# Kernel optimization log

Hardware: AMD Instinct MI355X
Metric: run time of the kernel (lower is better)

Reference implementation:

```python
import jax, jax.numpy as jnp
import numpy as np

B, T, E, H = 2, 4096, 768, 12
D = E // H  # head_dim = 64


def setup_inputs() -> dict:
    key = jax.random.key(0)
    ks = jax.random.split(key, 9)
    s = 1.0 / np.sqrt(E)
    return {
        "x": jax.random.normal(ks[0], (B, T, E), dtype=jnp.float32),
        "wq": jax.random.normal(ks[1], (E, E), dtype=jnp.float32) * s,
        "bq": jnp.zeros((E,), dtype=jnp.float32),
        "wk": jax.random.normal(ks[2], (E, E), dtype=jnp.float32) * s,
        "bk": jnp.zeros((E,), dtype=jnp.float32),
        "wv": jax.random.normal(ks[3], (E, E), dtype=jnp.float32) * s,
        "bv": jnp.zeros((E,), dtype=jnp.float32),
        "wo": jax.random.normal(ks[4], (E, E), dtype=jnp.float32) * s,
        "bo": jnp.zeros((E,), dtype=jnp.float32),
    }


def reference(x, wq, bq, wk, bk, wv, bv, wo, bo):
    # Linear projections (torch Linear: x @ W.T + b; weights here stored as (in,out))
    q = x @ wq + bq  # (B,T,E)
    k = x @ wk + bk
    v = x @ wv + bv

    def split(t):
        return t.reshape(B, T, H, D).transpose(0, 2, 1, 3)  # (B,H,T,D)

    q, k, v = split(q), split(k), split(v)
    scale = 1.0 / np.sqrt(D).astype(np.float32)
    scores = jnp.einsum("bhtd,bhsd->bhts", q, k) * scale  # (B,H,T,T)
    causal = jnp.tril(jnp.ones((T, T), dtype=bool))
    scores = jnp.where(causal, scores, -jnp.inf)
    attn = jax.nn.softmax(scores, axis=-1)
    out = jnp.einsum("bhts,bhsd->bhtd", attn, v)  # (B,H,T,D)
    out = out.transpose(0, 2, 1, 3).reshape(B, T, E)
    return out @ wo + bo
```

## Files before the change

### kernel.cpp

```cpp
#include <hip/hip_runtime.h>
#include <hip/hip_bf16.h>

#define TSEQ 4096
#define EMB 768
#define NH 12
#define DH 64
#define BT 8192
#define NROWS (24 * TSEQ)

typedef __attribute__((ext_vector_type(8))) short bf16x8;
typedef __attribute__((ext_vector_type(4))) float f32x4;

#define FENCE() asm volatile("" ::: "memory")

__device__ __forceinline__ f32x4 mfma16(bf16x8 a, bf16x8 b, f32x4 c) {
    return __builtin_amdgcn_mfma_f32_16x16x32_bf16(a, b, c, 0, 0, 0);
}

__device__ __forceinline__ void gload16(const void* g, void* l) {
    __builtin_amdgcn_global_load_lds((const __attribute__((address_space(1))) void*)g,
                                     (__attribute__((address_space(3))) void*)l, 16, 0, 0);
}

__global__ __launch_bounds__(256) void conv_all_k(const float* __restrict__ x,
                                                  __hip_bfloat16* __restrict__ xb,
                                                  const float* w0, const float* w1,
                                                  const float* w2, const float* w3,
                                                  __hip_bfloat16* o0, __hip_bfloat16* o1,
                                                  __hip_bfloat16* o2, __hip_bfloat16* o3) {
    __shared__ float tile[32][33];
    int bid = blockIdx.x;
    if (bid < 6144) {
        int i = (bid * 256 + threadIdx.x) * 4;
        float4 v = *(const float4*)(x + i);
        union { unsigned short u[4]; uint2 p; } o;
        __hip_bfloat16 t0 = __float2bfloat16(v.x); o.u[0] = *(unsigned short*)&t0;
        __hip_bfloat16 t1 = __float2bfloat16(v.y); o.u[1] = *(unsigned short*)&t1;
        __hip_bfloat16 t2 = __float2bfloat16(v.z); o.u[2] = *(unsigned short*)&t2;
        __hip_bfloat16 t3 = __float2bfloat16(v.w); o.u[3] = *(unsigned short*)&t3;
        *(uint2*)(xb + i) = o.p;
        return;
    }
    bid -= 6144;
    const int z = bid / 576, rr = bid % 576, by = rr / 24, bx = rr % 24;
    const float* w; __hip_bfloat16* o;
    switch (z) {
        case 0: w = w0; o = o0; break;
        case 1: w = w1; o = o1; break;
        case 2: w = w2; o = o2; break;
        default: w = w3; o = o3; break;
    }
    int tx = threadIdx.x & 31, ty = threadIdx.x >> 5;
    int kb = by * 32, nb = bx * 32;
    for (int i = 0; i < 32; i += 8)
        tile[ty + i][tx] = w[(size_t)(kb + ty + i) * EMB + nb + tx];
    __syncthreads();
    for (int i = 0; i < 32; i += 8)
        o[(size_t)(nb + ty + i) * EMB + kb + tx] = __float2bfloat16(tile[tx][ty + i]);
}

__device__ __forceinline__ void gemm_body(const __hip_bfloat16* __restrict__ A,
                                          const __hip_bfloat16* __restrict__ Wt,
                                          const float* __restrict__ bias,
                                          void* __restrict__ outp, int mode, float scale) {
    __shared__ alignas(16) char As[2][8192];
    __shared__ alignas(16) char Bs[2][8192];
    const int m0 = blockIdx.x * 128, n0 = blockIdx.y * 128;
    const int tid = threadIdx.x;
    const int lane = tid & 63, l15 = lane & 15, lg = lane >> 4;
    const int wave = tid >> 6, wm = wave >> 1, wn = wave & 1;
    const int swz = (l15 & 7) << 4;

    int mrow_[2]; int kelem_[2];
#pragma unroll
    for (int c = 0; c < 2; ++c) {
        int p = c * 4096 + tid * 16;
        int lrow = p >> 7, w = p & 127;
        int wp = w ^ ((lrow & 7) << 4);
        mrow_[c] = lrow + ((wp >> 6) & 1) * 64;
        kelem_[c] = (wp & 63) >> 1;
    }

    f32x4 acc[4][4];
    for (int i = 0; i < 4; ++i)
        for (int j = 0; j < 4; ++j) acc[i][j] = (f32x4){0.f, 0.f, 0.f, 0.f};

    auto stage = [&](int buf, int k0) {
#pragma unroll
        for (int c = 0; c < 2; ++c)
            gload16(A + (size_t)(m0 + mrow_[c]) * EMB + k0 + kelem_[c],
                    As[buf] + c * 4096 + wave * 1024);
#pragma unroll
        for (int c = 0; c < 2; ++c)
            gload16(Wt + (size_t)(n0 + mrow_[c]) * EMB + k0 + kelem_[c],
                    Bs[buf] + c * 4096 + wave * 1024);
    };

    stage(0, 0);
    const int NK = EMB / 32;
    for (int ks = 0; ks < NK; ++ks) {
        const int cur = ks & 1;
        asm volatile("s_waitcnt vmcnt(0)" ::: "memory");
        FENCE(); __builtin_amdgcn_s_barrier(); FENCE();
        if (ks + 1 < NK) stage(cur ^ 1, (ks + 1) * 32);
        bf16x8 af[4], bfv[4];
#pragma unroll
        for (int f = 0; f < 4; ++f)
            af[f] = *(const bf16x8*)(As[cur] + (f * 16 + l15) * 128 + ((wm * 64 + lg * 16) ^ swz));
#pragma unroll
        for (int f = 0; f < 4; ++f)
            bfv[f] = *(const bf16x8*)(Bs[cur] + (f * 16 + l15) * 128 + ((wn * 64 + lg * 16) ^ swz));
        __builtin_amdgcn_s_setprio(1);
#pragma unroll
        for (int i = 0; i < 4; ++i)
#pragma unroll
            for (int j = 0; j < 4; ++j)
                acc[i][j] = mfma16(af[i], bfv[j], acc[i][j]);
        __builtin_amdgcn_s_setprio(0);
    }

#pragma unroll
    for (int i = 0; i < 4; ++i) {
#pragma unroll
        for (int j = 0; j < 4; ++j) {
            const int n = n0 + wn * 64 + j * 16 + l15;
            const float bv = bias[n];
            const int mbase = m0 + wm * 64 + i * 16 + lg * 4;
#pragma unroll
            for (int r = 0; r < 4; ++r) {
                const int m = mbase + r;
                const float val = (acc[i][j][r] + bv) * scale;
                if (mode == 2) {
                    ((float*)outp)[(size_t)m * EMB + n] = val;
                } else {
                    const int b = m >> 12, t = m & (TSEQ - 1);
                    const int h = n >> 6, d = n & 63;
                    size_t addr;
                    if (mode == 0) addr = ((size_t)(b * NH + h) * TSEQ + t) * DH + d;
                    else           addr = ((size_t)(b * NH + h) * DH + d) * TSEQ + t;
                    ((__hip_bfloat16*)outp)[addr] = __float2bfloat16(val);
                }
            }
        }
    }
}

__global__ __launch_bounds__(256) void qkv_k(const __hip_bfloat16* __restrict__ xb,
                                             const __hip_bfloat16* __restrict__ wqT,
                                             const __hip_bfloat16* __restrict__ wkT,
                                             const __hip_bfloat16* __restrict__ wvT,
                                             const float* __restrict__ bq,
                                             const float* __restrict__ bk,
                                             const float* __restrict__ bv,
                                             __hip_bfloat16* __restrict__ qo,
                                             __hip_bfloat16* __restrict__ ko,
                                             __hip_bfloat16* __restrict__ vo) {
    const __hip_bfloat16* Wt; const float* bias; void* o; int mode; float scale;
    const float cq = 0.125f * 1.44269504089f;
    switch (blockIdx.z) {
        case 0:  Wt = wqT; bias = bq; o = qo; mode = 0; scale = cq;  break;
        case 1:  Wt = wkT; bias = bk; o = ko; mode = 0; scale = 1.f; break;
        default: Wt = wvT; bias = bv; o = vo; mode = 1; scale = 1.f; break;
    }
    gemm_body(xb, Wt, bias, o, mode, scale);
}

__global__ __launch_bounds__(256) void oproj64_k(const __hip_bfloat16* __restrict__ A,
                                                 const __hip_bfloat16* __restrict__ Wt,
                                                 const float* __restrict__ bias,
                                                 float* __restrict__ out) {
    __shared__ alignas(16) char As[2][4096];
    __shared__ alignas(16) char Bs[2][8192];
    const int m0 = blockIdx.x * 64, n0 = blockIdx.y * 128;
    const int tid = threadIdx.x;
    const int lane = tid & 63, l15 = lane & 15, lg = lane >> 4;
    const int wave = tid >> 6, wm = wave >> 1, wn = wave & 1;
    const int swz = (l15 & 7) << 4;

    int amrow, akelem;
    {
        int p = tid * 16;
        int lrow = p >> 7, w = p & 127;
        int wp = w ^ ((lrow & 7) << 4);
        amrow = lrow + ((wp >> 6) & 1) * 32;
        akelem = (wp & 63) >> 1;
    }
    int bnrow[2], bkelem[2];
#pragma unroll
    for (int c = 0; c < 2; ++c) {
        int p = c * 4096 + tid * 16;
        int lrow = p >> 7, w = p & 127;
        int wp = w ^ ((lrow & 7) << 4);
        bnrow[c] = lrow + ((wp >> 6) & 1) * 64;
        bkelem[c] = (wp & 63) >> 1;
    }

    f32x4 acc[2][4];
    for (int i = 0; i < 2; ++i)
        for (int j = 0; j < 4; ++j) acc[i][j] = (f32x4){0.f, 0.f, 0.f, 0.f};

    auto stage = [&](int buf, int k0) {
        gload16(A + (size_t)(m0 + amrow) * EMB + k0 + akelem,
                As[buf] + wave * 1024);
#pragma unroll
        for (int c = 0; c < 2; ++c)
            gload16(Wt + (size_t)(n0 + bnrow[c]) * EMB + k0 + bkelem[c],
                    Bs[buf] + c * 4096 + wave * 1024);
    };

    stage(0, 0);
    const int NK = EMB / 32;
    for (int ks = 0; ks < NK; ++ks) {
        const int cur = ks & 1;
        asm volatile("s_waitcnt vmcnt(0)" ::: "memory");
        FENCE(); __builtin_amdgcn_s_barrier(); FENCE();
        if (ks + 1 < NK) stage(cur ^ 1, (ks + 1) * 32);
        bf16x8 af[2], bfv[4];
#pragma unroll
        for (int f = 0; f < 2; ++f)
            af[f] = *(const bf16x8*)(As[cur] + (f * 16 + l15) * 128 + ((wm * 64 + lg * 16) ^ swz));
#pragma unroll
        for (int f = 0; f < 4; ++f)
            bfv[f] = *(const bf16x8*)(Bs[cur] + (f * 16 + l15) * 128 + ((wn * 64 + lg * 16) ^ swz));
        __builtin_amdgcn_s_setprio(1);
#pragma unroll
        for (int i = 0; i < 2; ++i)
#pragma unroll
            for (int j = 0; j < 4; ++j)
                acc[i][j] = mfma16(af[i], bfv[j], acc[i][j]);
        __builtin_amdgcn_s_setprio(0);
    }

#pragma unroll
    for (int i = 0; i < 2; ++i) {
#pragma unroll
        for (int j = 0; j < 4; ++j) {
            const int n = n0 + wn * 64 + j * 16 + l15;
            const float bv = bias[n];
            const int mbase = m0 + wm * 32 + i * 16 + lg * 4;
#pragma unroll
            for (int r = 0; r < 4; ++r)
                out[(size_t)(mbase + r) * EMB + n] = acc[i][j][r] + bv;
        }
    }
}

__global__ __launch_bounds__(256, 3) void attn_k(const __hip_bfloat16* __restrict__ qb,
                                                 const __hip_bfloat16* __restrict__ kb,
                                                 const __hip_bfloat16* __restrict__ vt,
                                                 __hip_bfloat16* __restrict__ opart,
                                                 float* __restrict__ lpart) {
    __shared__ alignas(16) char Ks[8192];
    __shared__ alignas(16) char Vs[8192];
    __shared__ alignas(16) char pbuf[4][2048];
    const int lane = threadIdx.x & 63, l15 = lane & 15, lg = lane >> 4;
    const int wave = threadIdx.x >> 6;
    const int bid = blockIdx.x;
    const int xcd = bid & 7, slot = bid >> 3;
    const int pair = slot & 31;
    const int parity = (slot >> 5) & 1;
    const int hgrp = slot >> 6;
    const int bh = xcd + hgrp * 8;
    const __hip_bfloat16* Qh = qb + (size_t)bh * TSEQ * DH;
    const __hip_bfloat16* Kh = kb + (size_t)bh * TSEQ * DH;
    const __hip_bfloat16* Vh = vt + (size_t)bh * DH * TSEQ;
    char* Pb = pbuf[wave];
    const int swz = (l15 & 7) << 4;
    const float M0 = 12.0f;

    bf16x8 ones8;
#pragma unroll
    for (int j = 0; j < 8; ++j) ones8[j] = (short)0x3F80;

    unsigned ka[8];
#pragma unroll
    for (int st = 0; st < 4; ++st)
#pragma unroll
        for (int ks = 0; ks < 2; ++ks)
            ka[st * 2 + ks] = (unsigned)((st * 16 + l15) * 128 + ((ks * 64 + lg * 16) ^ swz));
    char* pw[4]; char* pr[2];
#pragma unroll
    for (int st = 0; st < 4; ++st) pw[st] = Pb + l15 * 128 + ((st * 32 + lg * 8) ^ swz);
#pragma unroll
    for (int ks = 0; ks < 2; ++ks) pr[ks] = Pb + l15 * 128 + ((ks * 64 + lg * 16) ^ swz);
    const int dthr = wave * 16 + l15 - lg * 4;

    int r_[2], wp_[2];
#pragma unroll
    for (int c = 0; c < 2; ++c) {
        int p = c * 4096 + wave * 1024 + lane * 16;
        int r = p >> 7, w = p & 127;
        r_[c] = r;
        wp_[c] = (w ^ ((r & 7) << 4)) >> 1;
    }

    const int lo = pair, hi = 63 - pair;
    const int q0l = lo * 64 + wave * 16;
    const int q0h = hi * 64 + wave * 16;
    const int nsb = hi + 1;

    bf16x8 qh0 = *(const bf16x8*)(Qh + (size_t)(q0h + l15) * DH + lg * 8);
    bf16x8 qh1 = *(const bf16x8*)(Qh + (size_t)(q0h + l15) * DH + 32 + lg * 8);
    bf16x8 ql0 = *(const bf16x8*)(Qh + (size_t)(q0l + l15) * DH + lg * 8);
    bf16x8 ql1 = *(const bf16x8*)(Qh + (size_t)(q0l + l15) * DH + 32 + lg * 8);

    f32x4 oh[4], ol[4];
#pragma unroll
    for (int dt = 0; dt < 4; ++dt) { oh[dt] = (f32x4){0.f,0.f,0.f,0.f}; ol[dt] = (f32x4){0.f,0.f,0.f,0.f}; }
    f32x4 lh = (f32x4){0.f,0.f,0.f,0.f}, ll = (f32x4){0.f,0.f,0.f,0.f};

    const char* kg0 = (const char*)(Kh + (size_t)r_[0] * DH + wp_[0]) + parity * 8192;
    const char* kg1 = (const char*)(Kh + (size_t)r_[1] * DH + wp_[1]) + parity * 8192;
    const char* vg0 = (const char*)(Vh + (size_t)r_[0] * TSEQ + wp_[0]) + parity * 128;
    const char* vg1 = (const char*)(Vh + (size_t)r_[1] * TSEQ + wp_[1]) + parity * 128;

#define STAGE() do {                                                             \
    gload16(kg0, Ks + wave * 1024);                                              \
    gload16(kg1, Ks + 4096 + wave * 1024);                                       \
    gload16(vg0, Vs + wave * 1024);                                              \
    gload16(vg1, Vs + 4096 + wave * 1024);                                       \
    kg0 += 16384; kg1 += 16384; vg0 += 256; vg1 += 256;                          \
} while (0)

#define QKSM(KF, Q0, Q1, MASKB) do {                                             \
    f32x4 sa[4];                                                                 \
    __builtin_amdgcn_s_setprio(1);                                               \
    _Pragma("unroll")                                                            \
    for (int st = 0; st < 4; ++st) {                                             \
        f32x4 z = (f32x4){0.f, 0.f, 0.f, 0.f};                                   \
        z = mfma16(KF[st * 2 + 0], Q0, z);                                       \
        z = mfma16(KF[st * 2 + 1], Q1, z);                                       \
        sa[st] = z;                                                              \
    }                                                                            \
    __builtin_amdgcn_s_setprio(0);                                               \
    if (MASKB) {                                                                 \
        _Pragma("unroll")                                                        \
        for (int st = 0; st < 4; ++st)                                           \
            _Pragma("unroll")                                                    \
            for (int r = 0; r < 4; ++r)                                          \
                if (st * 16 + r > dthr) sa[st][r] = -INFINITY;                   \
    }                                                                            \
    _Pragma("unroll")                                                            \
    for (int st = 0; st < 4; ++st) {                                             \
        const float e0 = exp2f(sa[st][0] - M0);                                  \
        const float e1 = exp2f(sa[st][1] - M0);                                  \
        const float e2 = exp2f(sa[st][2] - M0);                                  \
        const float e3 = exp2f(sa[st][3] - M0);                                  \
        uint2 pkv;                                                               \
        asm("v_cvt_pk_bf16_f32 %0, %1, %2" : "=v"(pkv.x) : "v"(e0), "v"(e1));    \
        asm("v_cvt_pk_bf16_f32 %0, %1, %2" : "=v"(pkv.y) : "v"(e2), "v"(e3));    \
        *(uint2*)pw[st] = pkv;                                                   \
    }                                                                            \
} while (0)

#define PVU(VF, OV, LA) do {                                                     \
    bf16x8 pf0 = *(const bf16x8*)pr[0];                                          \
    bf16x8 pf1 = *(const bf16x8*)pr[1];                                          \
    __builtin_amdgcn_s_setprio(1);                                               \
    LA = mfma16(pf0, ones8, LA);                                                 \
    LA = mfma16(pf1, ones8, LA);                                                 \
    _Pragma("unroll")                                                            \
    for (int dt = 0; dt < 4; ++dt)                                               \
        OV[dt] = mfma16(pf0, VF[dt * 2 + 0], OV[dt]);                            \
    _Pragma("unroll")                                                            \
    for (int dt = 0; dt < 4; ++dt)                                               \
        OV[dt] = mfma16(pf1, VF[dt * 2 + 1], OV[dt]);                            \
    __builtin_amdgcn_s_setprio(0);                                               \
} while (0)

    STAGE();
    for (int sb = parity; sb < nsb; sb += 2) {
        const bool loact = (sb <= lo);
        asm volatile("s_waitcnt vmcnt(0)" ::: "memory");
        FENCE(); __builtin_amdgcn_s_barrier(); FENCE();
        bf16x8 kf[8];
#pragma unroll
        for (int i = 0; i < 8; ++i) kf[i] = *(const bf16x8*)(Ks + ka[i]);
        QKSM(kf, qh0, qh1, (sb == hi));
        bf16x8 vf[8];
#pragma unroll
        for (int i = 0; i < 8; ++i) vf[i] = *(const bf16x8*)(Vs + ka[i]);
        asm volatile("s_waitcnt lgkmcnt(0)" ::: "memory");
        FENCE(); __builtin_amdgcn_s_barrier(); FENCE();
        if (sb + 2 < nsb) STAGE();
        PVU(vf, oh, lh);
        if (loact) {
            FENCE();
            QKSM(kf, ql0, ql1, (sb == lo));
            asm volatile("s_waitcnt lgkmcnt(0)" ::: "memory");
            PVU(vf, ol, ll);
        }
    }

#undef PVU
#undef QKSM
#undef STAGE

    const size_t prow = ((size_t)parity * 24 + bh) * TSEQ;
    {
#pragma unroll
        for (int r = 0; r < 4; ++r) {
            const size_t base = (prow + q0h + lg * 4 + r) * DH;
#pragma unroll
            for (int dt = 0; dt < 4; ++dt)
                opart[base + dt * 16 + l15] = __float2bfloat16(oh[dt][r]);
        }
        if (l15 == 0) {
#pragma unroll
            for (int r = 0; r < 4; ++r) lpart[prow + q0h + lg * 4 + r] = lh[r];
        }
    }
    {
#pragma unroll
        for (int r = 0; r < 4; ++r) {
            const size_t base = (prow + q0l + lg * 4 + r) * DH;
#pragma unroll
            for (int dt = 0; dt < 4; ++dt)
                opart[base + dt * 16 + l15] = __float2bfloat16(ol[dt][r]);
        }
        if (l15 == 0) {
#pragma unroll
            for (int r = 0; r < 4; ++r) lpart[prow + q0l + lg * 4 + r] = ll[r];
        }
    }
}

__global__ __launch_bounds__(256) void comb_k(const __hip_bfloat16* __restrict__ opart,
                                              const float* __restrict__ lpart,
                                              __hip_bfloat16* __restrict__ ab) {
    const int idx = blockIdx.x * 256 + threadIdx.x;
    const int row = idx >> 3;
    const int d0 = (idx & 7) * 8;
    const int bh = row >> 12, qrow = row & 4095;
    const int b_ = bh / NH, h = bh % NH;
    bf16x8 a0 = *(const bf16x8*)(opart + (size_t)row * DH + d0);
    bf16x8 a1 = *(const bf16x8*)(opart + ((size_t)NROWS + row) * DH + d0);
    const float linv = 1.0f / (lpart[row] + lpart[NROWS + row]);
    union { unsigned short u[8]; uint4 v; } o;
#pragma unroll
    for (int j = 0; j < 8; ++j) {
        const float v0 = __uint_as_float(((unsigned)(unsigned short)a0[j]) << 16);
        const float v1 = __uint_as_float(((unsigned)(unsigned short)a1[j]) << 16);
        __hip_bfloat16 hb = __float2bfloat16((v0 + v1) * linv);
        o.u[j] = *(unsigned short*)&hb;
    }
    *(uint4*)(ab + ((size_t)(b_ * TSEQ + qrow)) * EMB + h * DH + d0) = o.v;
}

extern "C" void kernel_launch(void* const* d_in, const int* in_sizes, int n_in,
                              void* d_out, int out_size, void* d_ws, size_t ws_size,
                              hipStream_t stream) {
    (void)in_sizes; (void)n_in; (void)out_size; (void)ws_size;
    const float* x  = (const float*)d_in[0];
    const float* wq = (const float*)d_in[1];
    const float* bq = (const float*)d_in[2];
    const float* wk = (const float*)d_in[3];
    const float* bk = (const float*)d_in[4];
    const float* wv = (const float*)d_in[5];
    const float* bv = (const float*)d_in[6];
    const float* wo = (const float*)d_in[7];
    const float* bo = (const float*)d_in[8];
    float* out = (float*)d_out;

    char* ws = (char*)d_ws;
    size_t off = 0;
    auto alloc = [&](size_t bytes) {
        char* p = ws + off;
        off += (bytes + 255) & ~(size_t)255;
        return p;
    };
    __hip_bfloat16* xb   = (__hip_bfloat16*)alloc((size_t)BT * EMB * 2);
    __hip_bfloat16* qbf  = (__hip_bfloat16*)alloc((size_t)BT * EMB * 2);
    __hip_bfloat16* kbf  = (__hip_bfloat16*)alloc((size_t)BT * EMB * 2);
    __hip_bfloat16* vtb  = (__hip_bfloat16*)alloc((size_t)BT * EMB * 2);
    __hip_bfloat16* abf  = (__hip_bfloat16*)alloc((size_t)BT * EMB * 2);
    __hip_bfloat16* wqT  = (__hip_bfloat16*)alloc((size_t)EMB * EMB * 2);
    __hip_bfloat16* wkT  = (__hip_bfloat16*)alloc((size_t)EMB * EMB * 2);
    __hip_bfloat16* wvT  = (__hip_bfloat16*)alloc((size_t)EMB * EMB * 2);
    __hip_bfloat16* woT  = (__hip_bfloat16*)alloc((size_t)EMB * EMB * 2);
    __hip_bfloat16* opart = (__hip_bfloat16*)alloc((size_t)2 * NROWS * DH * 2);
    float*          lpart = (float*)alloc((size_t)2 * NROWS * 4);

    conv_all_k<<<6144 + 2304, 256, 0, stream>>>(x, xb, wq, wk, wv, wo, wqT, wkT, wvT, woT);
    qkv_k<<<dim3(64, 6, 3), 256, 0, stream>>>(xb, wqT, wkT, wvT, bq, bk, bv, qbf, kbf, vtb);
    attn_k<<<1536, 256, 0, stream>>>(qbf, kbf, vtb, opart, lpart);
    comb_k<<<NROWS * 8 / 256, 256, 0, stream>>>(opart, lpart, abf);
    oproj64_k<<<dim3(128, 6), 256, 0, stream>>>(abf, woT, bo, out);
}
```

Before: 183.7 us.

## Fuse split-KV combine into output projection and double-buffer K/V in attention

Removes the separate combine kernel: the output-projection GEMM now loads both partial attention outputs and their row sums, normalizes them, packs to bf16 and writes the A tile to LDS itself. This skips the write and re-read of the intermediate attention buffer and one launch. The cost is that the combine work is repeated for each of the 6 output column tiles, and the A tile now goes through registers instead of a direct global-to-LDS load. Separately, the attention kernel double-buffers its K/V LDS tiles, which removes the second barrier per iteration so the next block's loads can overlap compute, at the price of extra LDS that may reduce occupancy.

Measured after the change: 187.4 us. +2.0%, slower.

```diff
diff --git a/kernel.cpp b/kernel.cpp
--- a/kernel.cpp
+++ b/kernel.cpp
@@ -20,6 +20,10 @@
 __device__ __forceinline__ void gload16(const void* g, void* l) {
     __builtin_amdgcn_global_load_lds((const __attribute__((address_space(1))) void*)g,
                                      (__attribute__((address_space(3))) void*)l, 16, 0, 0);
+}
+
+__device__ __forceinline__ float bf2f(unsigned short u) {
+    return __uint_as_float(((unsigned)u) << 16);
 }
 
 __global__ __launch_bounds__(256) void conv_all_k(const float* __restrict__ x,
@@ -165,10 +169,11 @@
     gemm_body(xb, Wt, bias, o, mode, scale);
 }
 
-__global__ __launch_bounds__(256) void oproj64_k(const __hip_bfloat16* __restrict__ A,
-                                                 const __hip_bfloat16* __restrict__ Wt,
-                                                 const float* __restrict__ bias,
-                                                 float* __restrict__ out) {
+__global__ __launch_bounds__(256) void oprojc_k(const __hip_bfloat16* __restrict__ opart,
+                                                const float* __restrict__ lpart,
+                                                const __hip_bfloat16* __restrict__ Wt,
+                                                const float* __restrict__ bias,
+                                                float* __restrict__ out) {
     __shared__ alignas(16) char As[2][4096];
     __shared__ alignas(16) char Bs[2][8192];
     const int m0 = blockIdx.x * 64, n0 = blockIdx.y * 128;
@@ -185,6 +190,8 @@
         amrow = lrow + ((wp >> 6) & 1) * 32;
         akelem = (wp & 63) >> 1;
     }
+    const int m = m0 + amrow;
+    const int b_ = m >> 12, t = m & (TSEQ - 1);
     int bnrow[2], bkelem[2];
 #pragma unroll
     for (int c = 0; c < 2; ++c) {
@@ -200,8 +207,20 @@
         for (int j = 0; j < 4; ++j) acc[i][j] = (f32x4){0.f, 0.f, 0.f, 0.f};
 
     auto stage = [&](int buf, int k0) {
-        gload16(A + (size_t)(m0 + amrow) * EMB + k0 + akelem,
-                As[buf] + wave * 1024);
+        const int h = k0 >> 6;
+        const int d0 = (k0 & 63) + akelem;
+        const size_t orow = ((size_t)(b_ * NH + h)) * TSEQ + t;
+        bf16x8 a0 = *(const bf16x8*)(opart + orow * DH + d0);
+        bf16x8 a1 = *(const bf16x8*)(opart + ((size_t)NROWS + orow) * DH + d0);
+        const float li = 1.0f / (lpart[orow] + lpart[NROWS + orow]);
+        union { unsigned w[4]; uint4 v; } pk;
+#pragma unroll
+        for (int jp = 0; jp < 4; ++jp) {
+            const float e0 = (bf2f((unsigned short)a0[2 * jp]) + bf2f((unsigned short)a1[2 * jp])) * li;
+            const float e1 = (bf2f((unsigned short)a0[2 * jp + 1]) + bf2f((unsigned short)a1[2 * jp + 1])) * li;
+            asm("v_cvt_pk_bf16_f32 %0, %1, %2" : "=v"(pk.w[jp]) : "v"(e0), "v"(e1));
+        }
+        *(uint4*)(As[buf] + wave * 1024 + lane * 16) = pk.v;
 #pragma unroll
         for (int c = 0; c < 2; ++c)
             gload16(Wt + (size_t)(n0 + bnrow[c]) * EMB + k0 + bkelem[c],
@@ -212,7 +231,7 @@
     const int NK = EMB / 32;
     for (int ks = 0; ks < NK; ++ks) {
         const int cur = ks & 1;
-        asm volatile("s_waitcnt vmcnt(0)" ::: "memory");
+        asm volatile("s_waitcnt vmcnt(0) lgkmcnt(0)" ::: "memory");
         FENCE(); __builtin_amdgcn_s_barrier(); FENCE();
         if (ks + 1 < NK) stage(cur ^ 1, (ks + 1) * 32);
         bf16x8 af[2], bfv[4];
@@ -250,8 +269,8 @@
                                                  const __hip_bfloat16* __restrict__ vt,
                                                  __hip_bfloat16* __restrict__ opart,
                                                  float* __restrict__ lpart) {
-    __shared__ alignas(16) char Ks[8192];
-    __shared__ alignas(16) char Vs[8192];
+    __shared__ alignas(16) char Ks[2][8192];
+    __shared__ alignas(16) char Vs[2][8192];
     __shared__ alignas(16) char pbuf[4][2048];
     const int lane = threadIdx.x & 63, l15 = lane & 15, lg = lane >> 4;
     const int wave = threadIdx.x >> 6;
@@ -314,11 +333,11 @@
     const char* vg0 = (const char*)(Vh + (size_t)r_[0] * TSEQ + wp_[0]) + parity * 128;
     const char* vg1 = (const char*)(Vh + (size_t)r_[1] * TSEQ + wp_[1]) + parity * 128;
 
-#define STAGE() do {                                                             \
-    gload16(kg0, Ks + wave * 1024);                                              \
-    gload16(kg1, Ks + 4096 + wave * 1024);                                       \
-    gload16(vg0, Vs + wave * 1024);                                              \
-    gload16(vg1, Vs + 4096 + wave * 1024);                                       \
+#define STAGE(DST) do {                                                          \
+    gload16(kg0, Ks[DST] + wave * 1024);                                         \
+    gload16(kg1, Ks[DST] + 4096 + wave * 1024);                                  \
+    gload16(vg0, Vs[DST] + wave * 1024);                                         \
+    gload16(vg1, Vs[DST] + 4096 + wave * 1024);                                  \
     kg0 += 16384; kg1 += 16384; vg0 += 256; vg1 += 256;                          \
 } while (0)
 
@@ -368,21 +387,21 @@
     __builtin_amdgcn_s_setprio(0);                                               \
 } while (0)
 
-    STAGE();
+    STAGE(0);
+    int cur = 0;
     for (int sb = parity; sb < nsb; sb += 2) {
         const bool loact = (sb <= lo);
         asm volatile("s_waitcnt vmcnt(0)" ::: "memory");
         FENCE(); __builtin_amdgcn_s_barrier(); FENCE();
+        if (sb + 2 < nsb) STAGE(cur ^ 1);
         bf16x8 kf[8];
 #pragma unroll
-        for (int i = 0; i < 8; ++i) kf[i] = *(const bf16x8*)(Ks + ka[i]);
+        for (int i = 0; i < 8; ++i) kf[i] = *(const bf16x8*)(Ks[cur] + ka[i]);
         QKSM(kf, qh0, qh1, (sb == hi));
         bf16x8 vf[8];
 #pragma unroll
-        for (int i = 0; i < 8; ++i) vf[i] = *(const bf16x8*)(Vs + ka[i]);
+        for (int i = 0; i < 8; ++i) vf[i] = *(const bf16x8*)(Vs[cur] + ka[i]);
         asm volatile("s_waitcnt lgkmcnt(0)" ::: "memory");
-        FENCE(); __builtin_amdgcn_s_barrier(); FENCE();
-        if (sb + 2 < nsb) STAGE();
         PVU(vf, oh, lh);
         if (loact) {
             FENCE();
@@ -390,6 +409,7 @@
             asm volatile("s_waitcnt lgkmcnt(0)" ::: "memory");
             PVU(vf, ol, ll);
         }
+        cur ^= 1;
     }
 
 #undef PVU
@@ -423,28 +443,6 @@
             for (int r = 0; r < 4; ++r) lpart[prow + q0l + lg * 4 + r] = ll[r];
         }
     }
-}
-
-__global__ __launch_bounds__(256) void comb_k(const __hip_bfloat16* __restrict__ opart,
-                                              const float* __restrict__ lpart,
-                                              __hip_bfloat16* __restrict__ ab) {
-    const int idx = blockIdx.x * 256 + threadIdx.x;
-    const int row = idx >> 3;
-    const int d0 = (idx & 7) * 8;
-    const int bh = row >> 12, qrow = row & 4095;
-    const int b_ = bh / NH, h = bh % NH;
-    bf16x8 a0 = *(const bf16x8*)(opart + (size_t)row * DH + d0);
-    bf16x8 a1 = *(const bf16x8*)(opart + ((size_t)NROWS + row) * DH + d0);
-    const float linv = 1.0f / (lpart[row] + lpart[NROWS + row]);
-    union { unsigned short u[8]; uint4 v; } o;
-#pragma unroll
-    for (int j = 0; j < 8; ++j) {
-        const float v0 = __uint_as_float(((unsigned)(unsigned short)a0[j]) << 16);
-        const float v1 = __uint_as_float(((unsigned)(unsigned short)a1[j]) << 16);
-        __hip_bfloat16 hb = __float2bfloat16((v0 + v1) * linv);
-        o.u[j] = *(unsigned short*)&hb;
-    }
-    *(uint4*)(ab + ((size_t)(b_ * TSEQ + qrow)) * EMB + h * DH + d0) = o.v;
 }
 
 extern "C" void kernel_launch(void* const* d_in, const int* in_sizes, int n_in,
@@ -473,7 +471,6 @@
     __hip_bfloat16* qbf  = (__hip_bfloat16*)alloc((size_t)BT * EMB * 2);
     __hip_bfloat16* kbf  = (__hip_bfloat16*)alloc((size_t)BT * EMB * 2);
     __hip_bfloat16* vtb  = (__hip_bfloat16*)alloc((size_t)BT * EMB * 2);
-    __hip_bfloat16* abf  = (__hip_bfloat16*)alloc((size_t)BT * EMB * 2);
     __hip_bfloat16* wqT  = (__hip_bfloat16*)alloc((size_t)EMB * EMB * 2);
     __hip_bfloat16* wkT  = (__hip_bfloat16*)alloc((size_t)EMB * EMB * 2);
     __hip_bfloat16* wvT  = (__hip_bfloat16*)alloc((size_t)EMB * EMB * 2);
@@ -484,6 +481,5 @@
     conv_all_k<<<6144 + 2304, 256, 0, stream>>>(x, xb, wq, wk, wv, wo, wqT, wkT, wvT, woT);
     qkv_k<<<dim3(64, 6, 3), 256, 0, stream>>>(xb, wqT, wkT, wvT, bq, bk, bv, qbf, kbf, vtb);
     attn_k<<<1536, 256, 0, stream>>>(qbf, kbf, vtb, opart, lpart);
-    comb_k<<<NROWS * 8 / 256, 256, 0, stream>>>(opart, lpart, abf);
-    oproj64_k<<<dim3(128, 6), 256, 0, stream>>>(abf, woT, bo, out);
-}
+    oprojc_k<<<dim3(128, 6), 256, 0, stream>>>(opart, lpart, woT, bo, out);
+}
```
